# Performance work log

Hardware: AMD Instinct MI355X
Metric: run time of the kernel (lower is better)

The kernel has to match this reference:

```python
import jax, jax.numpy as jnp
import numpy as np

B, N, C = 16, 2048, 512
EPS = 1e-9        # numerical_stabilizer
BN_EPS = 1e-5     # flax BatchNorm default epsilon


def setup_inputs() -> dict:
    key = jax.random.key(0)
    ks = jax.random.split(key, 9)
    s = 1.0 / np.sqrt(C)

    def w(k):
        return jax.random.normal(k, (C, C), jnp.float32) * s

    return {
        "x": jax.random.normal(ks[0], (B, N, C), jnp.float32),
        "Wq": w(ks[1]), "bq": jnp.zeros((C,), jnp.float32),
        "Wk": w(ks[2]), "bk": jnp.zeros((C,), jnp.float32),
        "Wv": w(ks[3]), "bv": jnp.zeros((C,), jnp.float32),
        "Wo": w(ks[4]), "bo": jnp.zeros((C,), jnp.float32),
        "bn_scale": jnp.ones((C,), jnp.float32),
        "bn_bias": jnp.zeros((C,), jnp.float32),
        "bn_mean": jnp.zeros((C,), jnp.float32),
        "bn_var": jnp.ones((C,), jnp.float32),
    }


def reference(x, Wq, bq, Wk, bk, Wv, bv, Wo, bo,
              bn_scale, bn_bias, bn_mean, bn_var):
    # 1x1 'Conv' projections == pointwise linear layers
    q = x @ Wq + bq                                   # [B,N,C]
    k = x @ Wk + bk
    v = x @ Wv + bv

    # attention scores + row softmax
    att = jax.nn.softmax(jnp.einsum('bmc,bnc->bmn', q, k), axis=-1)  # [B,M,N]

    # post-softmax column renormalization: A / (eps + sum_M A),
    # then einsum '...MN,...NC->...NC' contracts M, so the effective
    # per-point scale is colsum / (eps + colsum).
    col = jnp.sum(att, axis=1)                        # [B,N]
    scale = col / (EPS + col)                         # [B,N]
    out = scale[..., None] * v                        # [B,N,C]

    # attention_type == 'naive': no offset
    y = out @ Wo + bo
    # BatchNorm with running stats (train=False)
    y = (y - bn_mean) * jax.lax.rsqrt(bn_var + BN_EPS) * bn_scale + bn_bias
    return jax.nn.relu(y) + x
```

## Files before the change

### kernel.cpp

```cpp
#include <hip/hip_runtime.h>
#include <math.h>

#define BB 16
#define NN 2048
#define CC 512
#define MM (BB * NN)
#define NSPLIT 4

typedef _Float16 half8 __attribute__((ext_vector_type(8)));
typedef _Float16 half4 __attribute__((ext_vector_type(4)));
typedef float floatx4 __attribute__((ext_vector_type(4)));

#define GLD16(gp, lp) __builtin_amdgcn_global_load_lds( \
    (const __attribute__((address_space(1))) void*)(gp), \
    (__attribute__((address_space(3))) void*)(lp), 16, 0, 0)

__device__ __forceinline__ int foff(int row16base, int fr, int g4) {
    return (row16base + fr) * 32 + ((g4 ^ ((fr >> 1) & 3)) << 3);
}

__global__ __launch_bounds__(256)
void split_x(const float* __restrict__ x, _Float16* __restrict__ xh,
             _Float16* __restrict__ xl)
{
    const size_t i = ((size_t)blockIdx.x * 256 + threadIdx.x) * 4;
    const float4 v = *(const float4*)(x + i);
    half4 h, l;
    h[0] = (_Float16)v.x; l[0] = (_Float16)(v.x - (float)h[0]);
    h[1] = (_Float16)v.y; l[1] = (_Float16)(v.y - (float)h[1]);
    h[2] = (_Float16)v.z; l[2] = (_Float16)(v.z - (float)h[2]);
    h[3] = (_Float16)v.w; l[3] = (_Float16)(v.w - (float)h[3]);
    *(half4*)(xh + i) = h;
    *(half4*)(xl + i) = l;
}

__global__ __launch_bounds__(256)
void conv_wT(const float* __restrict__ W, _Float16* __restrict__ Wt)
{
    const int o = blockIdx.x * 256 + threadIdx.x;
    const int n = o >> 9, k = o & 511;
    Wt[o] = (_Float16)W[k * 512 + n];
}

__global__ __launch_bounds__(256)
void calc_w2(const float* __restrict__ Wk, const float* __restrict__ bq,
             float* __restrict__ w2)
{
    const int i = blockIdx.x * 256 + threadIdx.x;
    if (i < 512) {
        float s = 0.0f;
        for (int j = 0; j < 512; ++j) s += Wk[i * 512 + j] * bq[j];
        w2[i] = s;
    }
}

__global__ __launch_bounds__(256)
void calc_beta(const float* __restrict__ x, const float* __restrict__ w2,
               float* __restrict__ bet)
{
    const int w = threadIdx.x >> 6, lane = threadIdx.x & 63;
    const int m = blockIdx.x * 4 + w;
    const float* xr = x + (size_t)m * CC;
    float s = 0.0f;
    for (int c = lane; c < CC; c += 64) s += xr[c] * w2[c];
    for (int off = 1; off < 64; off <<= 1) s += __shfl_xor(s, off);
    if (lane == 0) bet[m] = s;
}

__global__ __launch_bounds__(256)
void gemm_nt_split(const float* __restrict__ A, const float* __restrict__ Bm,
                   _Float16* __restrict__ outh, _Float16* __restrict__ outl)
{
    __shared__ float As[16][64];
    __shared__ float Bs[16][64];
    const int t = threadIdx.x, tc = t & 15, tr = t >> 4;
    const int j0 = blockIdx.x * 64, i0 = blockIdx.y * 64;
    const int lm = t >> 2, lk4 = (t & 3) << 2;
    float acc[4][4] = {};
    for (int kt = 0; kt < 512; kt += 16) {
        const float4 xa = *(const float4*)(A + (size_t)(j0 + lm) * 512 + kt + lk4);
        As[lk4 + 0][lm] = xa.x; As[lk4 + 1][lm] = xa.y;
        As[lk4 + 2][lm] = xa.z; As[lk4 + 3][lm] = xa.w;
        const float4 xb = *(const float4*)(Bm + (size_t)(i0 + lm) * 512 + kt + lk4);
        Bs[lk4 + 0][lm] = xb.x; Bs[lk4 + 1][lm] = xb.y;
        Bs[lk4 + 2][lm] = xb.z; Bs[lk4 + 3][lm] = xb.w;
        __syncthreads();
#pragma unroll
        for (int k = 0; k < 16; ++k) {
            float av[4], bv[4];
            *(float4*)av = *(const float4*)&As[k][tr * 4];
            *(float4*)bv = *(const float4*)&Bs[k][tc * 4];
#pragma unroll
            for (int i = 0; i < 4; ++i)
#pragma unroll
                for (int j = 0; j < 4; ++j)
                    acc[i][j] = fmaf(av[i], bv[j], acc[i][j]);
        }
        __syncthreads();
    }
#pragma unroll
    for (int i = 0; i < 4; ++i) {
        const int row = j0 + tr * 4 + i;
#pragma unroll
        for (int j = 0; j < 4; ++j) {
            const int col = i0 + tc * 4 + j;
            const float y = acc[i][j];
            const _Float16 h = (_Float16)y;
            outh[row * 512 + col] = h;
            outl[row * 512 + col] = (_Float16)(y - (float)h);
        }
    }
}

template<bool SPLIT, int MODE>
__global__ __launch_bounds__(256)
void gemm16(const _Float16* __restrict__ Ah, const _Float16* __restrict__ Al,
            const _Float16* __restrict__ Bh, const _Float16* __restrict__ Bl,
            const float* __restrict__ bias, const float* __restrict__ colsc,
            const float* __restrict__ bn_scale, const float* __restrict__ bn_bias,
            const float* __restrict__ bn_mean, const float* __restrict__ bn_var,
            const float* __restrict__ xres,
            _Float16* __restrict__ oh, _Float16* __restrict__ ol,
            float* __restrict__ outf)
{
    __shared__ __align__(16) _Float16 sAh[128 * 32], sBh[128 * 32];
    __shared__ __align__(16) _Float16 sAl[128 * 32], sBl[128 * 32];

    const int t = threadIdx.x, lane = t & 63, w = t >> 6;
    const int m0 = blockIdx.x * 128, n0 = blockIdx.y * 128;
    const int lr4 = lane >> 2;
    const int sw8 = (((lane & 3) ^ ((lr4 >> 1) & 3)) << 3);
    const int fr = lane & 15, g4 = lane >> 4;
    const int wr = (w >> 1) * 64, wc = (w & 1) * 64;

    floatx4 acc[4][4];
#pragma unroll
    for (int i = 0; i < 4; ++i)
#pragma unroll
        for (int j = 0; j < 4; ++j) acc[i][j] = (floatx4){0.f, 0.f, 0.f, 0.f};

    for (int kt = 0; kt < CC; kt += 32) {
#pragma unroll
        for (int c = 0; c < 2; ++c) {
            const int r = w * 32 + c * 16;
            const size_t goA = (size_t)(m0 + r + lr4) * CC + kt + sw8;
            const size_t goB = (size_t)(n0 + r + lr4) * CC + kt + sw8;
            GLD16(Ah + goA, sAh + r * 32);
            GLD16(Bh + goB, sBh + r * 32);
            if constexpr (SPLIT) {
                GLD16(Al + goA, sAl + r * 32);
                GLD16(Bl + goB, sBl + r * 32);
            }
        }
        __syncthreads();

        half8 fa[4], fb[4], fal[4], fbl[4];
#pragma unroll
        for (int rt = 0; rt < 4; ++rt) {
            fa[rt] = *(const half8*)&sAh[foff(wr + rt * 16, fr, g4)];
            if constexpr (SPLIT) fal[rt] = *(const half8*)&sAl[foff(wr + rt * 16, fr, g4)];
        }
#pragma unroll
        for (int ct = 0; ct < 4; ++ct) {
            fb[ct] = *(const half8*)&sBh[foff(wc + ct * 16, fr, g4)];
            if constexpr (SPLIT) fbl[ct] = *(const half8*)&sBl[foff(wc + ct * 16, fr, g4)];
        }
#pragma unroll
        for (int rt = 0; rt < 4; ++rt)
#pragma unroll
            for (int ct = 0; ct < 4; ++ct) {
                acc[rt][ct] = __builtin_amdgcn_mfma_f32_16x16x32_f16(
                    fa[rt], fb[ct], acc[rt][ct], 0, 0, 0);
                if constexpr (SPLIT) {
                    acc[rt][ct] = __builtin_amdgcn_mfma_f32_16x16x32_f16(
                        fa[rt], fbl[ct], acc[rt][ct], 0, 0, 0);
                    acc[rt][ct] = __builtin_amdgcn_mfma_f32_16x16x32_f16(
                        fal[rt], fb[ct], acc[rt][ct], 0, 0, 0);
                }
            }
        __syncthreads();
    }

#pragma unroll
    for (int rt = 0; rt < 4; ++rt)
#pragma unroll
        for (int ct = 0; ct < 4; ++ct) {
            const int col = n0 + wc + ct * 16 + fr;
#pragma unroll
            for (int reg = 0; reg < 4; ++reg) {
                const int row = m0 + wr + rt * 16 + g4 * 4 + reg;
                float y = acc[rt][ct][reg];
                if constexpr (MODE == 0) {
                    const _Float16 h = (_Float16)y;
                    oh[(size_t)row * CC + col] = h;
                    ol[(size_t)row * CC + col] = (_Float16)(y - (float)h);
                } else if constexpr (MODE == 1) {
                    y = (y + bias[col]) * colsc[row];
                    oh[(size_t)row * CC + col] = (_Float16)y;
                } else {
                    y += bias[col];
                    y = (y - bn_mean[col]) * rsqrtf(bn_var[col] + 1e-5f)
                            * bn_scale[col] + bn_bias[col];
                    y = fmaxf(y, 0.0f) + xres[(size_t)row * CC + col];
                    outf[(size_t)row * CC + col] = y;
                }
            }
        }
}

__device__ __forceinline__ void attn_decode3(int& xt, int& b, int& sp) {
    const int h = blockIdx.x + (blockIdx.y << 4) + (blockIdx.z << 8);
    xt = (h >> 3) & 15;
    const int g = ((h >> 7) << 3) | (h & 7);
    b = g & 15;
    sp = g >> 4;
}
__device__ __forceinline__ void attn_decode_col(int& xt, int& b, int& sp) {
    const int h = blockIdx.x + (blockIdx.y << 3) + (blockIdx.z << 7);
    xt = (h >> 3) & 7;
    const int g = ((h >> 6) << 3) | (h & 7);
    b = g & 15;
    sp = g >> 4;
}

__global__ __launch_bounds__(256, 2)
void attn_rowstats(const _Float16* __restrict__ ah_, const _Float16* __restrict__ al_,
                   const _Float16* __restrict__ xh_,
                   const float* __restrict__ bet,
                   float* __restrict__ pm, float* __restrict__ pl)
{
    __shared__ __align__(16) _Float16 A0[128 * 32], A1[128 * 32], A2[128 * 32];
    __shared__ __align__(16) _Float16 X0[256 * 32], X1[256 * 32], X2[256 * 32];
    __shared__ float wm[4][64], wl[4][64];

    int xt, b, sp;
    attn_decode3(xt, b, sp);
    const int m0 = xt * 128;
    const int t = threadIdx.x, lane = t & 63, w = t >> 6;
    const int lr4 = lane >> 2;
    const int sw8 = (((lane & 3) ^ ((lr4 >> 1) & 3)) << 3);
    const int fr = lane & 15, g4 = lane >> 4;
    const int wr = (w >> 1) * 64, wc = (w & 1) * 128;
    const size_t bbase = (size_t)b * NN;

    float betA[8], betB[8];
#pragma unroll
    for (int ct = 0; ct < 8; ++ct) {
        betA[ct] = bet[bbase + sp * 512 +   0 + wc + ct * 16 + fr];
        betB[ct] = bet[bbase + sp * 512 + 256 + wc + ct * 16 + fr];
    }

    float m_st[4][4], l_st[4][4];
#pragma unroll
    for (int i = 0; i < 4; ++i)
#pragma unroll
        for (int j = 0; j < 4; ++j) { m_st[i][j] = -3.0e38f; l_st[i][j] = 0.0f; }

    floatx4 acc[4][8];
#pragma unroll
    for (int i = 0; i < 4; ++i)
#pragma unroll
        for (int j = 0; j < 8; ++j) acc[i][j] = (floatx4){0.f, 0.f, 0.f, 0.f};

    auto stage = [&](_Float16* Sa, _Float16* Sx, int gt) {
        const int nn0 = sp * 512 + (gt >> 4) * 256;
        const int nkt = (gt & 15) * 32;
#pragma unroll
        for (int c = 0; c < 2; ++c) {
            const int r = w * 32 + c * 16;
            GLD16(ah_ + (bbase + m0 + r + lr4) * CC + nkt + sw8, Sa + r * 32);
        }
#pragma unroll
        for (int c = 0; c < 4; ++c) {
            const int r = w * 64 + c * 16;
            GLD16(xh_ + (bbase + nn0 + r + lr4) * CC + nkt + sw8, Sx + r * 32);
        }
    };

    auto tile = [&](const _Float16* Ra, const _Float16* Rx,
                    _Float16* Sa, _Float16* Sx, int gt, int mode) {
        const int kt = (gt & 15) * 32;
        half8 fal[4];
#pragma unroll
        for (int rt = 0; rt < 4; ++rt)
            fal[rt] = *(const half8*)(al_ + (bbase + m0 + wr + rt * 16 + fr) * CC
                                      + kt + g4 * 8);
        if (mode == 0) stage(Sa, Sx, gt + 2);
        half8 fa[4];
#pragma unroll
        for (int rt = 0; rt < 4; ++rt)
            fa[rt] = *(const half8*)&Ra[foff(wr + rt * 16, fr, g4)];
#pragma unroll
        for (int hh = 0; hh < 2; ++hh) {
            half8 fb[4];
#pragma unroll
            for (int c4 = 0; c4 < 4; ++c4)
                fb[c4] = *(const half8*)&Rx[foff(wc + (hh * 4 + c4) * 16, fr, g4)];
            __builtin_amdgcn_s_setprio(1);
#pragma unroll
            for (int rt = 0; rt < 4; ++rt)
#pragma unroll
                for (int c4 = 0; c4 < 4; ++c4) {
                    acc[rt][hh * 4 + c4] = __builtin_amdgcn_mfma_f32_16x16x32_f16(
                        fa[rt], fb[c4], acc[rt][hh * 4 + c4], 0, 0, 0);
                    acc[rt][hh * 4 + c4] = __builtin_amdgcn_mfma_f32_16x16x32_f16(
                        fal[rt], fb[c4], acc[rt][hh * 4 + c4], 0, 0, 0);
                }
            __builtin_amdgcn_s_setprio(0);
        }
        if ((gt & 15) == 15) {
            const bool c1 = (gt >> 4) != 0;
#pragma unroll
            for (int rt = 0; rt < 4; ++rt)
#pragma unroll
                for (int reg = 0; reg < 4; ++reg) {
                    float v[8];
#pragma unroll
                    for (int ct = 0; ct < 8; ++ct)
                        v[ct] = acc[rt][ct][reg] + (c1 ? betB[ct] : betA[ct]);
                    float mx = v[0];
#pragma unroll
                    for (int ct = 1; ct < 8; ++ct) mx = fmaxf(mx, v[ct]);
                    const float mo = m_st[rt][reg];
                    const float mn = fmaxf(mo, mx);
                    float s = 0.0f;
#pragma unroll
                    for (int ct = 0; ct < 8; ++ct) s += __expf(v[ct] - mn);
                    l_st[rt][reg] = l_st[rt][reg] * __expf(mo - mn) + s;
                    m_st[rt][reg] = mn;
                }
#pragma unroll
            for (int i = 0; i < 4; ++i)
#pragma unroll
                for (int j = 0; j < 8; ++j) acc[i][j] = (floatx4){0.f, 0.f, 0.f, 0.f};
        }
        if (mode == 0)      asm volatile("s_waitcnt vmcnt(6)" ::: "memory");
        else if (mode == 1) asm volatile("s_waitcnt vmcnt(0)" ::: "memory");
        __builtin_amdgcn_s_barrier();
        asm volatile("" ::: "memory");
    };

    stage(A0, X0, 0);
    stage(A1, X1, 1);
    asm volatile("s_waitcnt vmcnt(6)" ::: "memory");
    __builtin_amdgcn_s_barrier();
    asm volatile("" ::: "memory");

#pragma unroll 1
    for (int u = 0; u < 10; ++u) {
        const int gt = u * 3;
        tile(A0, X0, A2, X2, gt,     0);
        tile(A1, X1, A0, X0, gt + 1, 0);
        tile(A2, X2, A1, X1, gt + 2, 0);
    }
    tile(A0, X0, nullptr, nullptr, 30, 1);
    tile(A1, X1, nullptr, nullptr, 31, 2);

#pragma unroll
    for (int rt = 0; rt < 4; ++rt)
#pragma unroll
        for (int reg = 0; reg < 4; ++reg) {
            float m = m_st[rt][reg], l = l_st[rt][reg];
#pragma unroll
            for (int off = 1; off < 16; off <<= 1) {
                const float mo = __shfl_xor(m, off);
                const float lo = __shfl_xor(l, off);
                const float mn = fmaxf(m, mo);
                l = l * __expf(m - mn) + lo * __expf(mo - mn);
                m = mn;
            }
            if (fr == 0) {
                wm[w][rt * 16 + g4 * 4 + reg] = m;
                wl[w][rt * 16 + g4 * 4 + reg] = l;
            }
        }
    __syncthreads();
    if (t < 128) {
        const int r = t & 63;
        const int wa = (t < 64) ? 0 : 2, wb = wa + 1;
        const float ma = wm[wa][r], mb = wm[wb][r];
        const float M = fmaxf(ma, mb);
        const float L = wl[wa][r] * __expf(ma - M) + wl[wb][r] * __expf(mb - M);
        pm[(size_t)sp * MM + bbase + m0 + t] = M;
        pl[(size_t)sp * MM + bbase + m0 + t] = L;
    }
}

__global__ __launch_bounds__(256)
void rho_merge(const float* __restrict__ pm, const float* __restrict__ pl,
               float* __restrict__ rho)
{
    const size_t i = (size_t)blockIdx.x * 256 + threadIdx.x;
    float M = pm[i];
#pragma unroll
    for (int s = 1; s < NSPLIT; ++s) M = fmaxf(M, pm[s * (size_t)MM + i]);
    float L = 0.0f;
#pragma unroll
    for (int s = 0; s < NSPLIT; ++s)
        L += pl[s * (size_t)MM + i] * __expf(pm[s * (size_t)MM + i] - M);
    rho[i] = M + __logf(L);
}

__global__ __launch_bounds__(256, 2)
void attn_colsum(const _Float16* __restrict__ ah_, const _Float16* __restrict__ al_,
                 const _Float16* __restrict__ xh_,
                 const float* __restrict__ bet, const float* __restrict__ rho,
                 float* __restrict__ pc)
{
    __shared__ __align__(16) _Float16 A0[128 * 32], A1[128 * 32], A2[128 * 32];
    __shared__ __align__(16) _Float16 X0[256 * 32], X1[256 * 32], X2[256 * 32];
    __shared__ float cred[4][128];

    int xt, b, sp;
    attn_decode_col(xt, b, sp);
    const int n0 = xt * 256;
    const int t = threadIdx.x, lane = t & 63, w = t >> 6;
    const int lr4 = lane >> 2;
    const int sw8 = (((lane & 3) ^ ((lr4 >> 1) & 3)) << 3);
    const int fr = lane & 15, g4 = lane >> 4;
    const int wr = (w >> 1) * 64, wc = (w & 1) * 128;
    const size_t bbase = (size_t)b * NN;

    float bet_r[8];
#pragma unroll
    for (int ct = 0; ct < 8; ++ct)
        bet_r[ct] = bet[bbase + n0 + wc + ct * 16 + fr];

    float csum[8] = {0.f, 0.f, 0.f, 0.f, 0.f, 0.f, 0.f, 0.f};
    floatx4 rr[4];
    floatx4 acc[4][8];
#pragma unroll
    for (int i = 0; i < 4; ++i)
#pragma unroll
        for (int j = 0; j < 8; ++j) acc[i][j] = (floatx4){0.f, 0.f, 0.f, 0.f};

    auto stage = [&](_Float16* Sa, _Float16* Sx, int gt) {
        const int nm0 = sp * 512 + (gt >> 4) * 128;
        const int nkt = (gt & 15) * 32;
#pragma unroll
        for (int c = 0; c < 2; ++c) {
            const int r = w * 32 + c * 16;
            GLD16(ah_ + (bbase + nm0 + r + lr4) * CC + nkt + sw8, Sa + r * 32);
        }
#pragma unroll
        for (int c = 0; c < 4; ++c) {
            const int r = w * 64 + c * 16;
            GLD16(xh_ + (bbase + n0 + r + lr4) * CC + nkt + sw8, Sx + r * 32);
        }
    };

    auto tile = [&](const _Float16* Ra, const _Float16* Rx,
                    _Float16* Sa, _Float16* Sx, int gt, int mode) {
        const int kt = (gt & 15) * 32;
        const int m0c = sp * 512 + (gt >> 4) * 128;
        if ((gt & 15) == 0) {
#pragma unroll
            for (int rt = 0; rt < 4; ++rt)
                rr[rt] = *(const floatx4*)&rho[bbase + m0c + wr + rt * 16 + g4 * 4];
        }
        half8 fal[4];
#pragma unroll
        for (int rt = 0; rt < 4; ++rt)
            fal[rt] = *(const half8*)(al_ + (bbase + m0c + wr + rt * 16 + fr) * CC
                                      + kt + g4 * 8);
        if (mode == 0) stage(Sa, Sx, gt + 2);
        half8 fa[4];
#pragma unroll
        for (int rt = 0; rt < 4; ++rt)
            fa[rt] = *(const half8*)&Ra[foff(wr + rt * 16, fr, g4)];
#pragma unroll
        for (int hh = 0; hh < 2; ++hh) {
            half8 fb[4];
#pragma unroll
            for (int c4 = 0; c4 < 4; ++c4)
                fb[c4] = *(const half8*)&Rx[foff(wc + (hh * 4 + c4) * 16, fr, g4)];
            __builtin_amdgcn_s_setprio(1);
#pragma unroll
            for (int rt = 0; rt < 4; ++rt)
#pragma unroll
                for (int c4 = 0; c4 < 4; ++c4) {
                    acc[rt][hh * 4 + c4] = __builtin_amdgcn_mfma_f32_16x16x32_f16(
                        fa[rt], fb[c4], acc[rt][hh * 4 + c4], 0, 0, 0);
                    acc[rt][hh * 4 + c4] = __builtin_amdgcn_mfma_f32_16x16x32_f16(
                        fal[rt], fb[c4], acc[rt][hh * 4 + c4], 0, 0, 0);
                }
            __builtin_amdgcn_s_setprio(0);
        }
        if ((gt & 15) == 15) {
#pragma unroll
            for (int rt = 0; rt < 4; ++rt)
#pragma unroll
                for (int reg = 0; reg < 4; ++reg) {
                    const float r = rr[rt][reg];
#pragma unroll
                    for (int ct = 0; ct < 8; ++ct)
                        csum[ct] += __expf(acc[rt][ct][reg] + bet_r[ct] - r);
                }
#pragma unroll
            for (int i = 0; i < 4; ++i)
#pragma unroll
                for (int j = 0; j < 8; ++j) acc[i][j] = (floatx4){0.f, 0.f, 0.f, 0.f};
        }
        if (mode == 0)      asm volatile("s_waitcnt vmcnt(6)" ::: "memory");
        else if (mode == 1) asm volatile("s_waitcnt vmcnt(0)" ::: "memory");
        __builtin_amdgcn_s_barrier();
        asm volatile("" ::: "memory");
    };

    stage(A0, X0, 0);
    stage(A1, X1, 1);
    asm volatile("s_waitcnt vmcnt(6)" ::: "memory");
    __builtin_amdgcn_s_barrier();
    asm volatile("" ::: "memory");

#pragma unroll 1
    for (int u = 0; u < 20; ++u) {
        const int gt = u * 3;
        tile(A0, X0, A2, X2, gt,     0);
        tile(A1, X1, A0, X0, gt + 1, 0);
        tile(A2, X2, A1, X1, gt + 2, 0);
    }
    tile(A0, X0, A2, X2, 60, 0);
    tile(A1, X1, A0, X0, 61, 0);
    tile(A2, X2, nullptr, nullptr, 62, 1);
    tile(A0, X0, nullptr, nullptr, 63, 2);

#pragma unroll
    for (int ct = 0; ct < 8; ++ct) {
        csum[ct] += __shfl_xor(csum[ct], 16);
        csum[ct] += __shfl_xor(csum[ct], 32);
    }
    if (lane < 16)
#pragma unroll
        for (int ct = 0; ct < 8; ++ct) cred[w][ct * 16 + lane] = csum[ct];
    __syncthreads();
    if (t < 256) {
        const int c = t & 127;
        const float s = (t < 128) ? (cred[0][c] + cred[2][c])
                                  : (cred[1][c] + cred[3][c]);
        pc[(size_t)sp * MM + bbase + n0 + t] = s;
    }
}

__global__ __launch_bounds__(256)
void colsc_merge(const float* __restrict__ pc, float* __restrict__ colsc)
{
    const size_t i = (size_t)blockIdx.x * 256 + threadIdx.x;
    float c = 0.0f;
#pragma unroll
    for (int s = 0; s < NSPLIT; ++s) c += pc[s * (size_t)MM + i];
    colsc[i] = c / (1e-9f + c);
}

extern "C" void kernel_launch(void* const* d_in, const int* in_sizes, int n_in,
                              void* d_out, int out_size, void* d_ws, size_t ws_size,
                              hipStream_t stream)
{
    const float* x        = (const float*)d_in[0];
    const float* Wq       = (const float*)d_in[1];
    const float* bq       = (const float*)d_in[2];
    const float* Wk       = (const float*)d_in[3];
    const float* bk       = (const float*)d_in[4];   (void)bk;
    const float* Wv       = (const float*)d_in[5];
    const float* bv       = (const float*)d_in[6];
    const float* Wo       = (const float*)d_in[7];
    const float* bo       = (const float*)d_in[8];
    const float* bn_scale = (const float*)d_in[9];
    const float* bn_bias  = (const float*)d_in[10];
    const float* bn_mean  = (const float*)d_in[11];
    const float* bn_var   = (const float*)d_in[12];
    float* out = (float*)d_out;

    const size_t MMC = (size_t)MM * CC;
    _Float16* xh = (_Float16*)d_ws;
    _Float16* xl = xh + MMC;
    _Float16* ah = xl + MMC;
    _Float16* al = ah + MMC;
    _Float16* th  = al;
    _Float16* Wvt = ah;
    _Float16* Wot = ah + 512 * 512;

    char* ob = (char*)d_out;
    _Float16* Pth = (_Float16*)(ob);
    _Float16* Ptl = (_Float16*)(ob + (1u << 19));
    float* w2     = (float*)(ob + (2u << 19));
    float* bet    = (float*)(ob + (2u << 19) + 8192);
    float* rho    = (float*)(ob + 1318912);
    float* colsc  = (float*)(ob + 1449984);
    float* pm     = (float*)(ob + 1581056);
    float* pl     = (float*)(ob + 2105344);
    float* pc     = (float*)(ob + 2629632);

    const dim3 blk(256);
    const dim3 g16(MM / 128, CC / 128);
    const dim3 grow(NN / 128, BB, NSPLIT);
    const dim3 gcol(NN / 256, BB, NSPLIT);

    split_x<<<MMC / (256 * 4), blk, 0, stream>>>(x, xh, xl);
    gemm_nt_split<<<dim3(8, 8), blk, 0, stream>>>(Wk, Wq, Pth, Ptl);
    calc_w2<<<2, blk, 0, stream>>>(Wk, bq, w2);
    calc_beta<<<MM / 4, blk, 0, stream>>>(x, w2, bet);

    gemm16<true, 0><<<g16, blk, 0, stream>>>(xh, xl, Pth, Ptl,
        nullptr, nullptr, nullptr, nullptr, nullptr, nullptr, nullptr,
        ah, al, nullptr);

    attn_rowstats<<<grow, blk, 0, stream>>>(ah, al, xh, bet, pm, pl);
    rho_merge<<<MM / 256, blk, 0, stream>>>(pm, pl, rho);
    attn_colsum<<<gcol, blk, 0, stream>>>(ah, al, xh, bet, rho, pc);
    colsc_merge<<<MM / 256, blk, 0, stream>>>(pc, colsc);

    conv_wT<<<1024, blk, 0, stream>>>(Wv, Wvt);
    gemm16<false, 1><<<g16, blk, 0, stream>>>(xh, nullptr, Wvt, nullptr,
        bv, colsc, nullptr, nullptr, nullptr, nullptr, nullptr,
        th, nullptr, nullptr);

    conv_wT<<<1024, blk, 0, stream>>>(Wo, Wot);
    gemm16<false, 2><<<g16, blk, 0, stream>>>(th, nullptr, Wot, nullptr,
        bo, nullptr, bn_scale, bn_bias, bn_mean, bn_var, x,
        nullptr, nullptr, out);
}
```

Baseline: 632.7 us.

## Triple-buffer gemm16 LDS pipeline with 128x256 tiles and direct-global low-part loads

Reworks gemm16 into a three-stage LDS ring that prefetches two k-tiles ahead, replacing full __syncthreads with vmcnt waits and raw barriers. The output tile per block grows from 128x128 to 128x256, and the grid halves along N. In the split path the low-half fragments are read straight from global memory into registers instead of staging them in LDS. It also adds setprio around the MFMA bursts and a 2-block occupancy hint. The goal is to hide global load latency and improve data reuse, at the cost of more registers (32 accumulators), uncoalesced-ish direct global fragment loads, and hand-counted vmcnt values that must match the issued loads.

```diff
diff --git a/kernel.cpp b/kernel.cpp
--- a/kernel.cpp
+++ b/kernel.cpp
@@ -113,7 +113,7 @@
 }
 
 template<bool SPLIT, int MODE>
-__global__ __launch_bounds__(256)
+__global__ __launch_bounds__(256, 2)
 void gemm16(const _Float16* __restrict__ Ah, const _Float16* __restrict__ Al,
             const _Float16* __restrict__ Bh, const _Float16* __restrict__ Bl,
             const float* __restrict__ bias, const float* __restrict__ colsc,
@@ -123,68 +123,106 @@
             _Float16* __restrict__ oh, _Float16* __restrict__ ol,
             float* __restrict__ outf)
 {
-    __shared__ __align__(16) _Float16 sAh[128 * 32], sBh[128 * 32];
-    __shared__ __align__(16) _Float16 sAl[128 * 32], sBl[128 * 32];
+    __shared__ __align__(16) _Float16 sA0[128 * 32], sA1[128 * 32], sA2[128 * 32];
+    __shared__ __align__(16) _Float16 sB0[256 * 32], sB1[256 * 32], sB2[256 * 32];
 
     const int t = threadIdx.x, lane = t & 63, w = t >> 6;
-    const int m0 = blockIdx.x * 128, n0 = blockIdx.y * 128;
+    const int m0 = blockIdx.x * 128, n0 = blockIdx.y * 256;
     const int lr4 = lane >> 2;
     const int sw8 = (((lane & 3) ^ ((lr4 >> 1) & 3)) << 3);
     const int fr = lane & 15, g4 = lane >> 4;
-    const int wr = (w >> 1) * 64, wc = (w & 1) * 64;
-
-    floatx4 acc[4][4];
+    const int wr = (w >> 1) * 64, wc = (w & 1) * 128;
+
+    floatx4 acc[4][8];
 #pragma unroll
     for (int i = 0; i < 4; ++i)
 #pragma unroll
-        for (int j = 0; j < 4; ++j) acc[i][j] = (floatx4){0.f, 0.f, 0.f, 0.f};
-
-    for (int kt = 0; kt < CC; kt += 32) {
+        for (int j = 0; j < 8; ++j) acc[i][j] = (floatx4){0.f, 0.f, 0.f, 0.f};
+
+    auto stage = [&](_Float16* Sa, _Float16* Sb, int gt) {
+        const int kt = gt * 32;
 #pragma unroll
         for (int c = 0; c < 2; ++c) {
             const int r = w * 32 + c * 16;
-            const size_t goA = (size_t)(m0 + r + lr4) * CC + kt + sw8;
-            const size_t goB = (size_t)(n0 + r + lr4) * CC + kt + sw8;
-            GLD16(Ah + goA, sAh + r * 32);
-            GLD16(Bh + goB, sBh + r * 32);
-            if constexpr (SPLIT) {
-                GLD16(Al + goA, sAl + r * 32);
-                GLD16(Bl + goB, sBl + r * 32);
-            }
-        }
-        __syncthreads();
-
-        half8 fa[4], fb[4], fal[4], fbl[4];
-#pragma unroll
-        for (int rt = 0; rt < 4; ++rt) {
-            fa[rt] = *(const half8*)&sAh[foff(wr + rt * 16, fr, g4)];
-            if constexpr (SPLIT) fal[rt] = *(const half8*)&sAl[foff(wr + rt * 16, fr, g4)];
-        }
-#pragma unroll
-        for (int ct = 0; ct < 4; ++ct) {
-            fb[ct] = *(const half8*)&sBh[foff(wc + ct * 16, fr, g4)];
-            if constexpr (SPLIT) fbl[ct] = *(const half8*)&sBl[foff(wc + ct * 16, fr, g4)];
-        }
+            GLD16(Ah + (size_t)(m0 + r + lr4) * CC + kt + sw8, Sa + r * 32);
+        }
+#pragma unroll
+        for (int c = 0; c < 4; ++c) {
+            const int r = w * 64 + c * 16;
+            GLD16(Bh + (size_t)(n0 + r + lr4) * CC + kt + sw8, Sb + r * 32);
+        }
+    };
+
+    auto tile = [&](const _Float16* Ra, const _Float16* Rb,
+                    _Float16* Sa, _Float16* Sb, int gt, int mode) {
+        const int kt = gt * 32;
+        half8 fal[4], fbl[8];
+        if constexpr (SPLIT) {
+#pragma unroll
+            for (int rt = 0; rt < 4; ++rt)
+                fal[rt] = *(const half8*)(Al + (size_t)(m0 + wr + rt * 16 + fr) * CC
+                                          + kt + g4 * 8);
+#pragma unroll
+            for (int ct = 0; ct < 8; ++ct)
+                fbl[ct] = *(const half8*)(Bl + (size_t)(n0 + wc + ct * 16 + fr) * CC
+                                          + kt + g4 * 8);
+        }
+        if (mode == 0) stage(Sa, Sb, gt + 2);
+        half8 fa[4];
 #pragma unroll
         for (int rt = 0; rt < 4; ++rt)
-#pragma unroll
-            for (int ct = 0; ct < 4; ++ct) {
-                acc[rt][ct] = __builtin_amdgcn_mfma_f32_16x16x32_f16(
-                    fa[rt], fb[ct], acc[rt][ct], 0, 0, 0);
-                if constexpr (SPLIT) {
+            fa[rt] = *(const half8*)&Ra[foff(wr + rt * 16, fr, g4)];
+#pragma unroll
+        for (int hh = 0; hh < 2; ++hh) {
+            half8 fb[4];
+#pragma unroll
+            for (int c4 = 0; c4 < 4; ++c4)
+                fb[c4] = *(const half8*)&Rb[foff(wc + (hh * 4 + c4) * 16, fr, g4)];
+            __builtin_amdgcn_s_setprio(1);
+#pragma unroll
+            for (int rt = 0; rt < 4; ++rt)
+#pragma unroll
+                for (int c4 = 0; c4 < 4; ++c4) {
+                    const int ct = hh * 4 + c4;
                     acc[rt][ct] = __builtin_amdgcn_mfma_f32_16x16x32_f16(
-                        fa[rt], fbl[ct], acc[rt][ct], 0, 0, 0);
-                    acc[rt][ct] = __builtin_amdgcn_mfma_f32_16x16x32_f16(
-                        fal[rt], fb[ct], acc[rt][ct], 0, 0, 0);
+                        fa[rt], fb[c4], acc[rt][ct], 0, 0, 0);
+                    if constexpr (SPLIT) {
+                        acc[rt][ct] = __builtin_amdgcn_mfma_f32_16x16x32_f16(
+                            fa[rt], fbl[ct], acc[rt][ct], 0, 0, 0);
+                        acc[rt][ct] = __builtin_amdgcn_mfma_f32_16x16x32_f16(
+                            fal[rt], fb[c4], acc[rt][ct], 0, 0, 0);
+                    }
                 }
-            }
-        __syncthreads();
-    }
+            __builtin_amdgcn_s_setprio(0);
+        }
+        if (mode == 0)      asm volatile("s_waitcnt vmcnt(6)" ::: "memory");
+        else if (mode == 1) asm volatile("s_waitcnt vmcnt(0)" ::: "memory");
+        __builtin_amdgcn_s_barrier();
+        asm volatile("" ::: "memory");
+    };
+
+    stage(sA0, sB0, 0);
+    stage(sA1, sB1, 1);
+    asm volatile("s_waitcnt vmcnt(6)" ::: "memory");
+    __builtin_amdgcn_s_barrier();
+    asm volatile("" ::: "memory");
+
+#pragma unroll 1
+    for (int u = 0; u < 4; ++u) {
+        const int gt = u * 3;
+        tile(sA0, sB0, sA2, sB2, gt,     0);
+        tile(sA1, sB1, sA0, sB0, gt + 1, 0);
+        tile(sA2, sB2, sA1, sB1, gt + 2, 0);
+    }
+    tile(sA0, sB0, sA2, sB2, 12, 0);
+    tile(sA1, sB1, sA0, sB0, 13, 0);
+    tile(sA2, sB2, nullptr, nullptr, 14, 1);
+    tile(sA0, sB0, nullptr, nullptr, 15, 2);
 
 #pragma unroll
     for (int rt = 0; rt < 4; ++rt)
 #pragma unroll
-        for (int ct = 0; ct < 4; ++ct) {
+        for (int ct = 0; ct < 8; ++ct) {
             const int col = n0 + wc + ct * 16 + fr;
 #pragma unroll
             for (int reg = 0; reg < 4; ++reg) {
@@ -592,7 +630,7 @@
     float* pc     = (float*)(ob + 2629632);
 
     const dim3 blk(256);
-    const dim3 g16(MM / 128, CC / 128);
+    const dim3 g16(MM / 128, CC / 256);
     const dim3 grow(NN / 128, BB, NSPLIT);
     const dim3 gcol(NN / 256, BB, NSPLIT);
 
```

Measured after the change: 671.7 us. 6.2% more time.
